# Kernel tuning notes

Measured on AMD Instinct MI355X. Metric: run time of the kernel, lower is better.

Reference implementation:

```python
import jax, jax.numpy as jnp
import numpy as np
import math

V, D, H, NL, L, B = 32000, 1024, 16, 6, 1024, 2
HD = D // H
EPS = 1e-5


def _positional(L, D):
    # matches torch: exp(arange(0,D,2) * -(log(1000)/D))
    div = jnp.exp(jnp.arange(0, D, 2, dtype=jnp.float32) * (-math.log(1000.0) / D))
    k = jnp.arange(L, dtype=jnp.float32)[:, None]
    pos = jnp.zeros((L, D), dtype=jnp.float32)
    pos = pos.at[:, 0::2].set(jnp.sin(k * div))
    pos = pos.at[:, 1::2].set(jnp.cos(k * div))
    return pos[None]  # [1, L, D]


def setup_inputs() -> dict:
    key = jax.random.key(0)
    ks = jax.random.split(key, 12)
    s = 0.02
    tokens = jax.random.randint(ks[0], (B, L), 0, V)
    emb = jax.random.normal(ks[1], (V, D), jnp.float32) * s
    pos = _positional(L, D)
    ln1_g = jnp.ones((NL, D), jnp.float32)
    ln1_b = jnp.zeros((NL, D), jnp.float32)
    ln2_g = jnp.ones((NL, D), jnp.float32)
    ln2_b = jnp.zeros((NL, D), jnp.float32)
    attn_w = jax.random.normal(ks[2], (NL, D, 3 * D), jnp.float32) * s
    attn_b = jnp.zeros((NL, 3 * D), jnp.float32)
    proj_w = jax.random.normal(ks[3], (NL, D, D), jnp.float32) * s
    proj_b = jnp.zeros((NL, D), jnp.float32)
    mlp_w1 = jax.random.normal(ks[4], (NL, D, 4 * D), jnp.float32) * s
    mlp_b1 = jnp.zeros((NL, 4 * D), jnp.float32)
    mlp_w2 = jax.random.normal(ks[5], (NL, 4 * D, D), jnp.float32) * s
    mlp_b2 = jnp.zeros((NL, D), jnp.float32)
    out_w = jax.random.normal(ks[6], (D, V), jnp.float32) * s
    return dict(tokens=tokens, pos=pos, emb=emb,
                ln1_g=ln1_g, ln1_b=ln1_b, ln2_g=ln2_g, ln2_b=ln2_b,
                attn_w=attn_w, attn_b=attn_b, proj_w=proj_w, proj_b=proj_b,
                mlp_w1=mlp_w1, mlp_b1=mlp_b1, mlp_w2=mlp_w2, mlp_b2=mlp_b2,
                out_w=out_w)


def _ln(x, g, b):
    mu = jnp.mean(x, -1, keepdims=True)
    var = jnp.mean(jnp.square(x - mu), -1, keepdims=True)
    return (x - mu) * jax.lax.rsqrt(var + EPS) * g + b


def _block(x, p, causal_mask):
    ln1_g, ln1_b, ln2_g, ln2_b, aw, ab, pw, pb, w1, b1, w2, b2 = p
    h = _ln(x, ln1_g, ln1_b)
    qkv = h @ aw + ab                      # [B, L, 3D]
    q, k, v = jnp.split(qkv, 3, axis=-1)
    Bc, Lc = x.shape[0], x.shape[1]
    q = q.reshape(Bc, Lc, H, HD)
    k = k.reshape(Bc, Lc, H, HD)
    v = v.reshape(Bc, Lc, H, HD)
    scores = jnp.einsum('blhd,bmhd->bhlm', q, k) * (1.0 / math.sqrt(HD))
    scores = jnp.where(causal_mask, scores, -jnp.inf)
    attn = jax.nn.softmax(scores, axis=-1)
    y = jnp.einsum('bhlm,bmhd->blhd', attn, v).reshape(Bc, Lc, D)
    x = x + (y @ pw + pb)
    r = _ln(x, ln2_g, ln2_b)
    # NOTE: original ModuleList order applies GELU AFTER the second linear
    r = jax.nn.gelu((r @ w1 + b1) @ w2 + b2, approximate=False)
    return x + r


def reference(tokens, pos, emb, ln1_g, ln1_b, ln2_g, ln2_b,
              attn_w, attn_b, proj_w, proj_b,
              mlp_w1, mlp_b1, mlp_w2, mlp_b2, out_w):
    x = emb[tokens] + pos                  # [B, L, D]
    Lc = x.shape[1]
    causal_mask = jnp.tril(jnp.ones((Lc, Lc), bool))[None, None]
    for i in range(NL):
        p = (ln1_g[i], ln1_b[i], ln2_g[i], ln2_b[i],
             attn_w[i], attn_b[i], proj_w[i], proj_b[i],
             mlp_w1[i], mlp_b1[i], mlp_w2[i], mlp_b2[i])
        x = _block(x, p, causal_mask)
    return x @ out_w                       # [B, L, V] logits
```

## Files before the change

### kernel.cpp

```cpp
#include <hip/hip_runtime.h>
#include <hip/hip_bf16.h>
#include <math.h>

typedef __bf16 bf16;
typedef __bf16 bf16x4 __attribute__((ext_vector_type(4)));
typedef __bf16 bf16x8 __attribute__((ext_vector_type(8)));
typedef float f32x4 __attribute__((ext_vector_type(4)));

__device__ __forceinline__ void gld_lds16(const void* g, void* l) {
    __builtin_amdgcn_global_load_lds(
        (const __attribute__((address_space(1))) unsigned int*)g,
        (__attribute__((address_space(3))) unsigned int*)l, 16, 0, 0);
}

#define VMW(n) asm volatile("s_waitcnt vmcnt(" #n ")" ::: "memory")
#define BARR() asm volatile("s_barrier" ::: "memory")

__global__ __launch_bounds__(256) void k_embed(const int* __restrict__ tok,
                                               const float* __restrict__ emb,
                                               const float* __restrict__ pos,
                                               float* __restrict__ x) {
    int row = blockIdx.x;
    int l = row & 1023;
    int tk = tok[row];
    const float4* e = (const float4*)(emb + (size_t)tk * 1024);
    const float4* p = (const float4*)(pos + (size_t)l * 1024);
    float4* o = (float4*)(x + (size_t)row * 1024);
    float4 a = e[threadIdx.x], b = p[threadIdx.x];
    o[threadIdx.x] = make_float4(a.x + b.x, a.y + b.y, a.z + b.z, a.w + b.w);
}

__global__ __launch_bounds__(256) void k_ln(const float* __restrict__ x,
                                            const float* __restrict__ g,
                                            const float* __restrict__ b,
                                            bf16* __restrict__ out) {
    int row = blockIdx.x;
    int t = threadIdx.x;
    const float4* xr = (const float4*)(x + (size_t)row * 1024);
    float4 v = xr[t];
    float s1 = v.x + v.y + v.z + v.w;
    float s2 = v.x * v.x + v.y * v.y + v.z * v.z + v.w * v.w;
#pragma unroll
    for (int o = 32; o; o >>= 1) { s1 += __shfl_down(s1, o); s2 += __shfl_down(s2, o); }
    __shared__ float ps1[4], ps2[4], stat[2];
    int lane = t & 63, wid = t >> 6;
    if (lane == 0) { ps1[wid] = s1; ps2[wid] = s2; }
    __syncthreads();
    if (t == 0) {
        float a1 = ps1[0] + ps1[1] + ps1[2] + ps1[3];
        float a2 = ps2[0] + ps2[1] + ps2[2] + ps2[3];
        float mu = a1 * (1.f / 1024.f);
        float var = a2 * (1.f / 1024.f) - mu * mu;
        stat[0] = mu; stat[1] = rsqrtf(var + 1e-5f);
    }
    __syncthreads();
    float mu = stat[0], rs = stat[1];
    const float4* gv = (const float4*)g;
    const float4* bv = (const float4*)b;
    float4 gg = gv[t], bb = bv[t];
    bf16x4 o4;
    o4[0] = (bf16)((v.x - mu) * rs * gg.x + bb.x);
    o4[1] = (bf16)((v.y - mu) * rs * gg.y + bb.y);
    o4[2] = (bf16)((v.z - mu) * rs * gg.z + bb.z);
    o4[3] = (bf16)((v.w - mu) * rs * gg.w + bb.w);
    *(bf16x4*)(out + (size_t)row * 1024 + t * 4) = o4;
}

__global__ __launch_bounds__(256) void k_cast(const float* __restrict__ x, bf16* __restrict__ o) {
    int i = blockIdx.x * 256 + threadIdx.x;
    float4 v = ((const float4*)x)[i];
    bf16x4 b;
    b[0] = (bf16)v.x; b[1] = (bf16)v.y; b[2] = (bf16)v.z; b[3] = (bf16)v.w;
    ((bf16x4*)o)[i] = b;
}

__device__ __forceinline__ void transpose64(const float* __restrict__ W,
                                            bf16* __restrict__ WT,
                                            int K, int N, int n0, int k0, int t,
                                            float (*tile)[65]) {
    int tx = t & 15, ty = t >> 4;
#pragma unroll
    for (int i = 0; i < 64; i += 16) {
        float4 v = *(const float4*)&W[(size_t)(k0 + ty + i) * N + n0 + tx * 4];
        tile[ty + i][tx * 4 + 0] = v.x;
        tile[ty + i][tx * 4 + 1] = v.y;
        tile[ty + i][tx * 4 + 2] = v.z;
        tile[ty + i][tx * 4 + 3] = v.w;
    }
    __syncthreads();
    int n = t >> 3, ks = t & 7;
#pragma unroll
    for (int pass = 0; pass < 2; ++pass) {
        int nn = n + pass * 32;
        bf16x8 v;
#pragma unroll
        for (int j = 0; j < 8; ++j) v[j] = (bf16)tile[ks * 8 + j][nn];
        *(bf16x8*)&WT[(size_t)(n0 + nn) * K + k0 + ks * 8] = v;
    }
}

__global__ __launch_bounds__(256) void k_transpose_layer(const float* __restrict__ aw,
                                                         const float* __restrict__ pw,
                                                         const float* __restrict__ m1,
                                                         const float* __restrict__ m2,
                                                         bf16* __restrict__ wT) {
    __shared__ float tile[64][65];
    int bid = blockIdx.x;
    const float* src; bf16* dst; int K, N, tn, tk;
    if (bid < 768)       { src = aw; dst = wT;            K = 1024; N = 3072; tn = bid % 48; tk = bid / 48; }
    else if (bid < 1024) { int b = bid - 768;  src = pw; dst = wT + 3145728; K = 1024; N = 1024; tn = b % 16; tk = b / 16; }
    else if (bid < 2048) { int b = bid - 1024; src = m1; dst = wT + 4194304; K = 1024; N = 4096; tn = b % 64; tk = b / 64; }
    else                 { int b = bid - 2048; src = m2; dst = wT + 8388608; K = 4096; N = 1024; tn = b % 16; tk = b / 16; }
    transpose64(src, dst, K, N, tn * 64, tk * 64, threadIdx.x, tile);
}

__global__ __launch_bounds__(256) void k_transpose_out(const float* __restrict__ W,
                                                       bf16* __restrict__ WT) {
    __shared__ float tile[64][65];
    int bid = blockIdx.x;
    int tn = bid % 500, tk = bid / 500;
    transpose64(W, WT, 1024, 32000, tn * 64, tk * 64, threadIdx.x, tile);
}

__device__ __forceinline__ void stage128(const char* Ab, const char* Bb,
                                         char* As, char* Bs, int Kb, int k0b, int t) {
#pragma unroll
    for (int j = 0; j < 4; ++j) {
        int idx = j * 256 + t;
        int row = idx >> 3;
        int cb = (idx & 7) << 4;
        int scb = cb ^ ((row & 7) << 4);
        gld_lds16(Ab + (size_t)row * Kb + k0b + scb, As + idx * 16);
        gld_lds16(Bb + (size_t)row * Kb + k0b + scb, Bs + idx * 16);
    }
}

template <int EPI>
__global__ __launch_bounds__(256) void k_gemm2(const bf16* __restrict__ A,
                                               const bf16* __restrict__ BT,
                                               const float* __restrict__ bias,
                                               const float* __restrict__ resid,
                                               float* __restrict__ outf,
                                               bf16* __restrict__ outb,
                                               int N, int K) {
    __shared__ __align__(16) bf16 As[2][128 * 64];
    __shared__ __align__(16) bf16 Bs[2][128 * 64];
    int per = gridDim.x >> 3;
    int tile = (blockIdx.x & 7) * per + (blockIdx.x >> 3);
    int bm = tile & 15, bn = tile >> 4;
    int t = threadIdx.x, lane = t & 63;
    int wr = t >> 7, wc = (t >> 6) & 1;
    f32x4 acc[4][4] = {};
    const char* Ab = (const char*)(A + (size_t)bm * 128 * K);
    const char* Bb = (const char*)(BT + (size_t)bn * 128 * K);
    int Kb = K * 2;
    int nk = K >> 6;
    stage128(Ab, Bb, (char*)As[0], (char*)Bs[0], Kb, 0, t);
    VMW(0); BARR();
    for (int tt = 0; tt < nk; ++tt) {
        int cur = tt & 1;
        if (tt + 1 < nk)
            stage128(Ab, Bb, (char*)As[cur ^ 1], (char*)Bs[cur ^ 1], Kb, (tt + 1) * 128, t);
        const char* Ac = (const char*)As[cur];
        const char* Bc = (const char*)Bs[cur];
#pragma unroll
        for (int kk = 0; kk < 2; ++kk) {
            bf16x8 af[4], bfr[4];
            int cb = kk * 64 + ((lane >> 4) << 4);
#pragma unroll
            for (int m = 0; m < 4; ++m) {
                int r = wr * 64 + m * 16 + (lane & 15);
                af[m] = *(const bf16x8*)(Ac + r * 128 + (cb ^ ((r & 7) << 4)));
            }
#pragma unroll
            for (int n = 0; n < 4; ++n) {
                int r = wc * 64 + n * 16 + (lane & 15);
                bfr[n] = *(const bf16x8*)(Bc + r * 128 + (cb ^ ((r & 7) << 4)));
            }
#pragma unroll
            for (int m = 0; m < 4; ++m)
#pragma unroll
                for (int n = 0; n < 4; ++n)
                    acc[m][n] = __builtin_amdgcn_mfma_f32_16x16x32_bf16(af[m], bfr[n], acc[m][n], 0, 0, 0);
        }
        VMW(0); BARR();
    }
    int row0 = bm * 128 + wr * 64 + ((lane >> 4) << 2);
    int col0 = bn * 128 + wc * 64 + (lane & 15);
#pragma unroll
    for (int m = 0; m < 4; ++m) {
#pragma unroll
        for (int n = 0; n < 4; ++n) {
            int col = col0 + n * 16;
            float bv = bias[col];
#pragma unroll
            for (int r = 0; r < 4; ++r) {
                int row = row0 + m * 16 + r;
                size_t idx = (size_t)row * N + col;
                float v = acc[m][n][r] + bv;
                if (EPI == 0) {
                    outb[idx] = (bf16)v;
                } else if (EPI == 1) {
                    outf[idx] = resid[idx] + v;
                } else {
                    outf[idx] = resid[idx] + 0.5f * v * (1.0f + erff(v * 0.70710678118f));
                }
            }
        }
    }
}

__device__ __forceinline__ void stage64(const char* Ab, const char* Bb,
                                        char* As, char* Bs, int Kb, int k0b, int t) {
#pragma unroll
    for (int j = 0; j < 2; ++j) {
        int idx = j * 256 + t;
        int row = idx >> 3;
        int cb = (idx & 7) << 4;
        int scb = cb ^ ((row & 7) << 4);
        gld_lds16(Ab + (size_t)row * Kb + k0b + scb, As + idx * 16);
        gld_lds16(Bb + (size_t)row * Kb + k0b + scb, Bs + idx * 16);
    }
}

template <int EPI>
__global__ __launch_bounds__(256) void k_gemm64(const bf16* __restrict__ A,
                                                const bf16* __restrict__ BT,
                                                const float* __restrict__ bias,
                                                const float* __restrict__ resid,
                                                float* __restrict__ outf,
                                                int N, int K) {
    __shared__ __align__(16) bf16 As[2][64 * 64];
    __shared__ __align__(16) bf16 Bs[2][64 * 64];
    int per = gridDim.x >> 3;
    int tile = (blockIdx.x & 7) * per + (blockIdx.x >> 3);
    int bm = tile & 31, bn = tile >> 5;
    int t = threadIdx.x, lane = t & 63, wid = t >> 6;
    f32x4 acc[4] = {};
    const char* Ab = (const char*)(A + (size_t)bm * 64 * K);
    const char* Bb = (const char*)(BT + (size_t)bn * 64 * K);
    int Kb = K * 2;
    int nk = K >> 6;
    stage64(Ab, Bb, (char*)As[0], (char*)Bs[0], Kb, 0, t);
    VMW(0); BARR();
    for (int tt = 0; tt < nk; ++tt) {
        int cur = tt & 1;
        if (tt + 1 < nk)
            stage64(Ab, Bb, (char*)As[cur ^ 1], (char*)Bs[cur ^ 1], Kb, (tt + 1) * 128, t);
        const char* Ac = (const char*)As[cur];
        const char* Bc = (const char*)Bs[cur];
#pragma unroll
        for (int kk = 0; kk < 2; ++kk) {
            int cb = kk * 64 + ((lane >> 4) << 4);
            int ra = wid * 16 + (lane & 15);
            bf16x8 af = *(const bf16x8*)(Ac + ra * 128 + (cb ^ ((ra & 7) << 4)));
            bf16x8 bfr[4];
#pragma unroll
            for (int n = 0; n < 4; ++n) {
                int r = n * 16 + (lane & 15);
                bfr[n] = *(const bf16x8*)(Bc + r * 128 + (cb ^ ((r & 7) << 4)));
            }
#pragma unroll
            for (int n = 0; n < 4; ++n)
                acc[n] = __builtin_amdgcn_mfma_f32_16x16x32_bf16(af, bfr[n], acc[n], 0, 0, 0);
        }
        VMW(0); BARR();
    }
    int row0 = bm * 64 + wid * 16 + ((lane >> 4) << 2);
    int col0 = bn * 64 + (lane & 15);
#pragma unroll
    for (int n = 0; n < 4; ++n) {
        int col = col0 + n * 16;
        float bv = bias[col];
#pragma unroll
        for (int r = 0; r < 4; ++r) {
            int row = row0 + r;
            size_t idx = (size_t)row * N + col;
            float v = acc[n][r] + bv;
            if (EPI == 1) {
                outf[idx] = resid[idx] + v;
            } else {
                outf[idx] = resid[idx] + 0.5f * v * (1.0f + erff(v * 0.70710678118f));
            }
        }
    }
}

__device__ __forceinline__ void stage_half256(const char* gtile, char* ldst,
                                              int Kb, int t) {
#pragma unroll
    for (int j = 0; j < 2; ++j) {
        int idx = j * 512 + t;
        int row = idx >> 3;
        int cb = (idx & 7) << 4;
        int scb = cb ^ ((row & 7) << 4);
        gld_lds16(gtile + (size_t)row * Kb + scb, ldst + idx * 16);
    }
}

template <int MH, int NH>
__device__ __forceinline__ void phase256(const bf16* Abuf, const bf16* Bbuf,
                                         int lane, int wm, int wn,
                                         f32x4 (&acc)[8][4]) {
    int lrow = lane & 15, lk = lane >> 4;
    bf16x8 af[4][2], bfr[2][2];
#pragma unroll
    for (int kk = 0; kk < 2; ++kk) {
        int cb = kk * 64 + lk * 16;
#pragma unroll
        for (int m = 0; m < 4; ++m) {
            int row = (MH * 4 + m) * 32 + wm * 16 + lrow;
            af[m][kk] = *(const bf16x8*)((const char*)Abuf + row * 128 + (cb ^ ((row & 7) << 4)));
        }
#pragma unroll
        for (int n = 0; n < 2; ++n) {
            int row = (NH * 2 + n) * 64 + wn * 16 + lrow;
            bfr[n][kk] = *(const bf16x8*)((const char*)Bbuf + row * 128 + (cb ^ ((row & 7) << 4)));
        }
    }
    __builtin_amdgcn_s_setprio(1);
#pragma unroll
    for (int kk = 0; kk < 2; ++kk)
#pragma unroll
        for (int m = 0; m < 4; ++m)
#pragma unroll
            for (int n = 0; n < 2; ++n)
                acc[MH * 4 + m][NH * 2 + n] = __builtin_amdgcn_mfma_f32_16x16x32_bf16(
                    af[m][kk], bfr[n][kk], acc[MH * 4 + m][NH * 2 + n], 0, 0, 0);
    __builtin_amdgcn_s_setprio(0);
    __builtin_amdgcn_sched_barrier(0);
}

__global__ __launch_bounds__(512, 2) void k_gemm256(const bf16* __restrict__ A,
                                                    const bf16* __restrict__ BT,
                                                    float* __restrict__ outf,
                                                    int N, int K) {
    __shared__ __align__(16) bf16 As[2][256 * 64];
    __shared__ __align__(16) bf16 Bs[2][256 * 64];
    int t = threadIdx.x, lane = t & 63, wid = t >> 6;
    int wm = wid >> 2, wn = wid & 3;
    int tile = (blockIdx.x & 7) * 125 + (blockIdx.x >> 3);
    int bm = tile & 7;
    int bn = tile >> 3;

    const char* Ab = (const char*)(A + (size_t)bm * 256 * K);
    const char* Bb = (const char*)(BT + (size_t)bn * 256 * K);
    int Kb = K * 2;
    f32x4 acc[8][4] = {};

    stage_half256(Ab, (char*)As[0], Kb, t);
    __builtin_amdgcn_sched_barrier(0);
    stage_half256(Bb, (char*)Bs[0], Kb, t);
    __builtin_amdgcn_sched_barrier(0);
    stage_half256(Bb + (size_t)128 * Kb, (char*)Bs[0] + 16384, Kb, t);
    __builtin_amdgcn_sched_barrier(0);
    stage_half256(Ab + (size_t)128 * Kb, (char*)As[0] + 16384, Kb, t);
    __builtin_amdgcn_sched_barrier(0);

    int nk = K >> 6;
    for (int tt = 0; tt < nk - 1; ++tt) {
        int cur = tt & 1, nxt = cur ^ 1;
        const bf16* Ac = As[cur];
        const bf16* Bc = Bs[cur];
        const char* Abn = Ab + (size_t)(tt + 1) * 128;
        const char* Bbn = Bb + (size_t)(tt + 1) * 128;
        stage_half256(Abn, (char*)As[nxt], Kb, t);
        VMW(6); BARR();
        phase256<0, 0>(Ac, Bc, lane, wm, wn, acc);
        BARR();
        stage_half256(Bbn, (char*)Bs[nxt], Kb, t);
        VMW(6); BARR();
        phase256<0, 1>(Ac, Bc, lane, wm, wn, acc);
        BARR();
        stage_half256(Bbn + (size_t)128 * Kb, (char*)Bs[nxt] + 16384, Kb, t);
        VMW(6); BARR();
        phase256<1, 0>(Ac, Bc, lane, wm, wn, acc);
        BARR();
        stage_half256(Abn + (size_t)128 * Kb, (char*)As[nxt] + 16384, Kb, t);
        phase256<1, 1>(Ac, Bc, lane, wm, wn, acc);
        BARR();
    }
    {
        int cur = (nk - 1) & 1;
        const bf16* Ac = As[cur];
        const bf16* Bc = Bs[cur];
        VMW(4); BARR();
        phase256<0, 0>(Ac, Bc, lane, wm, wn, acc);
        BARR();
        VMW(2); BARR();
        phase256<0, 1>(Ac, Bc, lane, wm, wn, acc);
        BARR();
        VMW(0); BARR();
        phase256<1, 0>(Ac, Bc, lane, wm, wn, acc);
        BARR();
        phase256<1, 1>(Ac, Bc, lane, wm, wn, acc);
    }

    size_t row0 = (size_t)bm * 256 + wm * 16 + (lane >> 4) * 4;
    int col0 = bn * 256 + wn * 16 + (lane & 15);
#pragma unroll
    for (int mi = 0; mi < 8; ++mi) {
#pragma unroll
        for (int ni = 0; ni < 4; ++ni) {
            int col = col0 + ni * 64;
#pragma unroll
            for (int r = 0; r < 4; ++r) {
                size_t row = row0 + mi * 32 + r;
                __builtin_nontemporal_store(acc[mi][ni][r], &outf[row * N + col]);
            }
        }
    }
}

__global__ __launch_bounds__(256) void k_attn(const bf16* __restrict__ qkv, bf16* __restrict__ y) {
    int tile = (blockIdx.x & 7) * 64 + (blockIdx.x >> 3);
    int qb = tile & 15;
    int bh = tile >> 4;
    int b = bh >> 4, h = bh & 15;
    int t = threadIdx.x, lane = t & 63, wid = t >> 6;
    int tok0 = b << 10;
    int q0 = qb << 6;
    __shared__ bf16 Qs[64][64];
    __shared__ bf16 Ks[64][64];
    __shared__ bf16 Vt[64][64];
    __shared__ bf16 Ps[4][16][64];
    const char* qbase = (const char*)qkv;
#pragma unroll
    for (int j = 0; j < 2; ++j) {
        int off = (j * 256 + t) * 16;
        int row = off >> 7, colb = off & 127;
        gld_lds16(qbase + ((size_t)(tok0 + q0 + row) * 3072 + h * 64) * 2 + colb, (char*)Qs + off);
    }
    asm volatile("s_waitcnt vmcnt(0)" ::: "memory");
    __syncthreads();
    int kof = (lane >> 4) << 3;
    bf16x8 aq0 = *(const bf16x8*)&Qs[wid * 16 + (lane & 15)][kof];
    bf16x8 aq1 = *(const bf16x8*)&Qs[wid * 16 + (lane & 15)][32 + kof];
    f32x4 o[4] = {};
    float mrun[4], lrun[4];
#pragma unroll
    for (int r = 0; r < 4; ++r) { mrun[r] = -INFINITY; lrun[r] = 0.f; }
    int qrow = q0 + wid * 16 + ((lane >> 4) << 2);

    for (int kv0 = 0; kv0 <= q0; kv0 += 64) {
        __syncthreads();
#pragma unroll
        for (int j = 0; j < 2; ++j) {
            int off = (j * 256 + t) * 16;
            int row = off >> 7, colb = off & 127;
            gld_lds16(qbase + ((size_t)(tok0 + kv0 + row) * 3072 + 1024 + h * 64) * 2 + colb,
                      (char*)Ks + off);
        }
        {
            int kv = t >> 2, d0 = (t & 3) * 16;
            const bf16* vrow = qkv + (size_t)(tok0 + kv0 + kv) * 3072 + 2048 + h * 64 + d0;
#pragma unroll
            for (int e4 = 0; e4 < 4; ++e4) {
                bf16x4 vv = *(const bf16x4*)(vrow + e4 * 4);
                Vt[d0 + e4 * 4 + 0][kv] = vv[0];
                Vt[d0 + e4 * 4 + 1][kv] = vv[1];
                Vt[d0 + e4 * 4 + 2][kv] = vv[2];
                Vt[d0 + e4 * 4 + 3][kv] = vv[3];
            }
        }
        asm volatile("s_waitcnt vmcnt(0)" ::: "memory");
        __syncthreads();
        f32x4 s[4];
#pragma unroll
        for (int n = 0; n < 4; ++n) {
            bf16x8 bk0 = *(const bf16x8*)&Ks[n * 16 + (lane & 15)][kof];
            bf16x8 bk1 = *(const bf16x8*)&Ks[n * 16 + (lane & 15)][32 + kof];
            f32x4 z = {};
            z = __builtin_amdgcn_mfma_f32_16x16x32_bf16(aq0, bk0, z, 0, 0, 0);
            z = __builtin_amdgcn_mfma_f32_16x16x32_bf16(aq1, bk1, z, 0, 0, 0);
            s[n] = z;
        }
        float mx[4];
#pragma unroll
        for (int r = 0; r < 4; ++r) mx[r] = -INFINITY;
#pragma unroll
        for (int n = 0; n < 4; ++n) {
            int col = kv0 + n * 16 + (lane & 15);
#pragma unroll
            for (int r = 0; r < 4; ++r) {
                float sv = s[n][r] * 0.125f;
                sv = (col <= qrow + r) ? sv : -INFINITY;
                s[n][r] = sv;
                mx[r] = fmaxf(mx[r], sv);
            }
        }
#pragma unroll
        for (int r = 0; r < 4; ++r)
#pragma unroll
            for (int m = 1; m < 16; m <<= 1) mx[r] = fmaxf(mx[r], __shfl_xor(mx[r], m));
        float scl[4];
#pragma unroll
        for (int r = 0; r < 4; ++r) {
            float mn = fmaxf(mrun[r], mx[r]);
            scl[r] = __expf(mrun[r] - mn);
            mrun[r] = mn;
        }
        float rs[4] = {0.f, 0.f, 0.f, 0.f};
#pragma unroll
        for (int n = 0; n < 4; ++n)
#pragma unroll
            for (int r = 0; r < 4; ++r) {
                float p = __expf(s[n][r] - mrun[r]);
                s[n][r] = p;
                rs[r] += p;
            }
#pragma unroll
        for (int r = 0; r < 4; ++r) {
#pragma unroll
            for (int m = 1; m < 16; m <<= 1) rs[r] += __shfl_xor(rs[r], m);
            lrun[r] = lrun[r] * scl[r] + rs[r];
        }
#pragma unroll
        for (int n = 0; n < 4; ++n)
#pragma unroll
            for (int r = 0; r < 4; ++r) {
                o[n][r] *= scl[r];
                Ps[wid][(lane >> 4) * 4 + r][n * 16 + (lane & 15)] = (bf16)s[n][r];
            }
        bf16x8 ap0 = *(const bf16x8*)&Ps[wid][lane & 15][kof];
        bf16x8 ap1 = *(const bf16x8*)&Ps[wid][lane & 15][32 + kof];
#pragma unroll
        for (int n = 0; n < 4; ++n) {
            bf16x8 bv0 = *(const bf16x8*)&Vt[n * 16 + (lane & 15)][kof];
            bf16x8 bv1 = *(const bf16x8*)&Vt[n * 16 + (lane & 15)][32 + kof];
            o[n] = __builtin_amdgcn_mfma_f32_16x16x32_bf16(ap0, bv0, o[n], 0, 0, 0);
            o[n] = __builtin_amdgcn_mfma_f32_16x16x32_bf16(ap1, bv1, o[n], 0, 0, 0);
        }
    }
#pragma unroll
    for (int n = 0; n < 4; ++n)
#pragma unroll
        for (int r = 0; r < 4; ++r) {
            int row = tok0 + qrow + r;
            y[(size_t)row * 1024 + h * 64 + n * 16 + (lane & 15)] = (bf16)(o[n][r] / lrun[r]);
        }
}

extern "C" void kernel_launch(void* const* d_in, const int* in_sizes, int n_in,
                              void* d_out, int out_size, void* d_ws, size_t ws_size,
                              hipStream_t stream) {
    const int*   tokens = (const int*)d_in[0];
    const float* pos    = (const float*)d_in[1];
    const float* emb    = (const float*)d_in[2];
    const float* ln1_g  = (const float*)d_in[3];
    const float* ln1_b  = (const float*)d_in[4];
    const float* ln2_g  = (const float*)d_in[5];
    const float* ln2_b  = (const float*)d_in[6];
    const float* attn_w = (const float*)d_in[7];
    const float* attn_b = (const float*)d_in[8];
    const float* proj_w = (const float*)d_in[9];
    const float* proj_b = (const float*)d_in[10];
    const float* mlp_w1 = (const float*)d_in[11];
    const float* mlp_b1 = (const float*)d_in[12];
    const float* mlp_w2 = (const float*)d_in[13];
    const float* mlp_b2 = (const float*)d_in[14];
    const float* out_w  = (const float*)d_in[15];
    float* out = (float*)d_out;

    char* ws = (char*)d_ws;
    size_t off = 0;
    auto alloc = [&](size_t bytes) {
        void* p = ws + off;
        off = (off + bytes + 255) & ~(size_t)255;
        return p;
    };
    float* x   = (float*)alloc((size_t)2048 * 1024 * 4);
    bf16* hb   = (bf16*)alloc((size_t)2048 * 1024 * 2);
    bf16* qkvb = (bf16*)alloc((size_t)2048 * 3072 * 2);
    bf16* yb   = (bf16*)alloc((size_t)2048 * 1024 * 2);
    bf16* hidb = (bf16*)alloc((size_t)2048 * 4096 * 2);
    bf16* wT   = (bf16*)alloc((size_t)32000 * 1024 * 2);

    k_embed<<<2048, 256, 0, stream>>>(tokens, emb, pos, x);

    for (int i = 0; i < 6; ++i) {
        k_transpose_layer<<<3072, 256, 0, stream>>>(
            attn_w + (size_t)i * 1024 * 3072, proj_w + (size_t)i * 1024 * 1024,
            mlp_w1 + (size_t)i * 1024 * 4096, mlp_w2 + (size_t)i * 4096 * 1024, wT);
        k_ln<<<2048, 256, 0, stream>>>(x, ln1_g + i * 1024, ln1_b + i * 1024, hb);
        k_gemm2<0><<<384, 256, 0, stream>>>(hb, wT, attn_b + i * 3072,
                                            nullptr, nullptr, qkvb, 3072, 1024);
        k_attn<<<512, 256, 0, stream>>>(qkvb, yb);
        k_gemm64<1><<<512, 256, 0, stream>>>(yb, wT + 3145728, proj_b + i * 1024,
                                             x, x, 1024, 1024);
        k_ln<<<2048, 256, 0, stream>>>(x, ln2_g + i * 1024, ln2_b + i * 1024, hb);
        k_gemm2<0><<<512, 256, 0, stream>>>(hb, wT + 4194304, mlp_b1 + i * 4096,
                                            nullptr, nullptr, hidb, 4096, 1024);
        k_gemm64<2><<<512, 256, 0, stream>>>(hidb, wT + 8388608, mlp_b2 + i * 1024,
                                             x, x, 1024, 4096);
    }

    k_cast<<<2048, 256, 0, stream>>>(x, hb);
    k_transpose_out<<<8000, 256, 0, stream>>>(out_w, wT);
    k_gemm256<<<1000, 512, 0, stream>>>(hb, wT, out, 32000, 1024);
}
```

Measured before the change: 1.289 ms.

## Restructure 256 GEMM pipeline with full-tile staging and triple-buffered B

Replaces the half-tile, phase-interleaved double-buffer pipeline with full-tile staging, A double-buffered and B triple-buffered two steps ahead, and fewer barriers per K-step. The larger LDS footprint drops occupancy to one block per CU. Output stores switch from nontemporal to regular stores. Intent is to cut barrier overhead and deepen prefetch, at the risk of less latency hiding from reduced occupancy.

```diff
diff --git a/kernel.cpp b/kernel.cpp
--- a/kernel.cpp
+++ b/kernel.cpp
@@ -286,10 +286,10 @@
     }
 }
 
-__device__ __forceinline__ void stage_half256(const char* gtile, char* ldst,
+__device__ __forceinline__ void stage_full256(const char* gtile, char* ldst,
                                               int Kb, int t) {
 #pragma unroll
-    for (int j = 0; j < 2; ++j) {
+    for (int j = 0; j < 4; ++j) {
         int idx = j * 512 + t;
         int row = idx >> 3;
         int cb = (idx & 7) << 4;
@@ -331,12 +331,12 @@
     __builtin_amdgcn_sched_barrier(0);
 }
 
-__global__ __launch_bounds__(512, 2) void k_gemm256(const bf16* __restrict__ A,
+__global__ __launch_bounds__(512, 1) void k_gemm256(const bf16* __restrict__ A,
                                                     const bf16* __restrict__ BT,
                                                     float* __restrict__ outf,
                                                     int N, int K) {
-    __shared__ __align__(16) bf16 As[2][256 * 64];
-    __shared__ __align__(16) bf16 Bs[2][256 * 64];
+    __shared__ __align__(16) bf16 Asb[2][256 * 64];
+    __shared__ __align__(16) bf16 Bsb[3][256 * 64];
     int t = threadIdx.x, lane = t & 63, wid = t >> 6;
     int wm = wid >> 2, wn = wid & 3;
     int tile = (blockIdx.x & 7) * 125 + (blockIdx.x >> 3);
@@ -346,53 +346,28 @@
     const char* Ab = (const char*)(A + (size_t)bm * 256 * K);
     const char* Bb = (const char*)(BT + (size_t)bn * 256 * K);
     int Kb = K * 2;
+    int nk = K >> 6;
     f32x4 acc[8][4] = {};
 
-    stage_half256(Ab, (char*)As[0], Kb, t);
-    __builtin_amdgcn_sched_barrier(0);
-    stage_half256(Bb, (char*)Bs[0], Kb, t);
-    __builtin_amdgcn_sched_barrier(0);
-    stage_half256(Bb + (size_t)128 * Kb, (char*)Bs[0] + 16384, Kb, t);
-    __builtin_amdgcn_sched_barrier(0);
-    stage_half256(Ab + (size_t)128 * Kb, (char*)As[0] + 16384, Kb, t);
-    __builtin_amdgcn_sched_barrier(0);
-
-    int nk = K >> 6;
-    for (int tt = 0; tt < nk - 1; ++tt) {
-        int cur = tt & 1, nxt = cur ^ 1;
-        const bf16* Ac = As[cur];
-        const bf16* Bc = Bs[cur];
-        const char* Abn = Ab + (size_t)(tt + 1) * 128;
-        const char* Bbn = Bb + (size_t)(tt + 1) * 128;
-        stage_half256(Abn, (char*)As[nxt], Kb, t);
-        VMW(6); BARR();
+    stage_full256(Ab, (char*)Asb[0], Kb, t);
+    stage_full256(Bb, (char*)Bsb[0], Kb, t);
+    stage_full256(Bb + 128, (char*)Bsb[1], Kb, t);
+    VMW(4);
+    BARR();
+
+    for (int tt = 0; tt < nk; ++tt) {
+        BARR();
+        int ka = (tt + 1 < nk) ? tt + 1 : nk - 1;
+        int kb = (tt + 2 < nk) ? tt + 2 : nk - 1;
+        stage_full256(Ab + (size_t)ka * 128, (char*)Asb[(tt + 1) & 1], Kb, t);
+        stage_full256(Bb + (size_t)kb * 128, (char*)Bsb[(tt + 2) % 3], Kb, t);
+        VMW(12);
+        BARR();
+        const bf16* Ac = Asb[tt & 1];
+        const bf16* Bc = Bsb[tt % 3];
         phase256<0, 0>(Ac, Bc, lane, wm, wn, acc);
-        BARR();
-        stage_half256(Bbn, (char*)Bs[nxt], Kb, t);
-        VMW(6); BARR();
         phase256<0, 1>(Ac, Bc, lane, wm, wn, acc);
-        BARR();
-        stage_half256(Bbn + (size_t)128 * Kb, (char*)Bs[nxt] + 16384, Kb, t);
-        VMW(6); BARR();
         phase256<1, 0>(Ac, Bc, lane, wm, wn, acc);
-        BARR();
-        stage_half256(Abn + (size_t)128 * Kb, (char*)As[nxt] + 16384, Kb, t);
-        phase256<1, 1>(Ac, Bc, lane, wm, wn, acc);
-        BARR();
-    }
-    {
-        int cur = (nk - 1) & 1;
-        const bf16* Ac = As[cur];
-        const bf16* Bc = Bs[cur];
-        VMW(4); BARR();
-        phase256<0, 0>(Ac, Bc, lane, wm, wn, acc);
-        BARR();
-        VMW(2); BARR();
-        phase256<0, 1>(Ac, Bc, lane, wm, wn, acc);
-        BARR();
-        VMW(0); BARR();
-        phase256<1, 0>(Ac, Bc, lane, wm, wn, acc);
-        BARR();
         phase256<1, 1>(Ac, Bc, lane, wm, wn, acc);
     }
 
@@ -406,7 +381,7 @@
 #pragma unroll
             for (int r = 0; r < 4; ++r) {
                 size_t row = row0 + mi * 32 + r;
-                __builtin_nontemporal_store(acc[mi][ni][r], &outf[row * N + col]);
+                outf[row * N + col] = acc[mi][ni][r];
             }
         }
     }
```

After: 1.275 ms. About the same (-1.1%).
